# Kernel optimization log

Measured on AMD Instinct MI355X. Metric: run time of the kernel, lower is better.

## Reference

```python
import jax, jax.numpy as jnp
import numpy as np

IN_F, OUT_F = 4096, 14336
F8_MAX = 448.0  # max magnitude of float8_e4m3fn


def setup_inputs() -> dict:
    key = jax.random.key(0)
    kx, kw, kb = jax.random.split(key, 3)
    x = jax.random.normal(kx, (2, 512, IN_F), dtype=jnp.bfloat16)
    w = jax.random.normal(kw, (OUT_F, IN_F), dtype=jnp.float32) * 0.02
    # per-tensor scale: amax / 448 (as in F8Linear.__init__)
    w_scale = (jnp.maximum(jnp.abs(w).max(), 1e-30) / F8_MAX).astype(jnp.float32)
    # quantize to fp8 e4m3; roundtrip back to float32 so the stored values are
    # exactly the fp8-representable values (float32 container keeps the bwd
    # reference's jax.vjp happy while the math is identical)
    w_f8 = jnp.clip(w / w_scale, -F8_MAX, F8_MAX).astype(jnp.float8_e4m3fn).astype(jnp.float32)
    bias = jax.random.normal(kb, (OUT_F,), dtype=jnp.float32) * 0.02
    return {"x": x, "weight_f8": w_f8, "w_scale": w_scale, "bias": bias}


def reference(x, weight_f8, w_scale, bias):
    # dequantize to activation dtype, then GEMM: y = x @ w^T + b
    w = weight_f8.astype(x.dtype) * w_scale.astype(x.dtype)   # [out, in]
    y = jnp.einsum('bsi,oi->bso', x, w) + bias.astype(x.dtype)
    return y
```

## Files before the change

kernel.cpp:

```cpp
#include <hip/hip_runtime.h>
#include <hip/hip_bf16.h>
#include <stdint.h>


#define IN_F   4096
#define OUT_F  14336
#define M_TOT  1024

#define BM 128
#define BN 128
#define BK 32
#define KTILES (IN_F / BK)

typedef __bf16  bf16x8 __attribute__((ext_vector_type(8)));
typedef __bf16  bf16x4 __attribute__((ext_vector_type(4)));
typedef float   f32x4  __attribute__((ext_vector_type(4)));

__device__ __forceinline__ void async_copy16(const void* g, void* l) {
    __builtin_amdgcn_global_load_lds(
        (const __attribute__((address_space(1))) void*)g,
        (__attribute__((address_space(3))) void*)l,
        16, 0, 0);
}

__global__ void detect_x_dtype(const uint32_t* __restrict__ xb,
                               int* __restrict__ flag) {
    __shared__ int any_low;
    if (threadIdx.x == 0) any_low = 0;
    __syncthreads();
    uint32_t bad = 0;
    for (int i = threadIdx.x; i < 1024; i += 256) bad |= (xb[i] & 0xFFFFu);
    if (bad) atomicOr(&any_low, 1);
    __syncthreads();
    if (threadIdx.x == 0) *flag = (any_low == 0) ? 1 : 0;
}

__global__ __launch_bounds__(256) void cvt_w_kernel(
    const f32x4* __restrict__ in, bf16x4* __restrict__ out) {
    const int stride = 3584 * 256;
    for (int i = blockIdx.x * 256 + threadIdx.x; i < 14680064; i += stride) {
        f32x4 v = in[i];
        bf16x4 o;
        o[0] = (__bf16)v[0]; o[1] = (__bf16)v[1];
        o[2] = (__bf16)v[2]; o[3] = (__bf16)v[3];
        out[i] = o;
    }
}

__global__ __launch_bounds__(256) void cvt_x_kernel(
    const void* __restrict__ xraw, bf16x4* __restrict__ out,
    const int* __restrict__ flag) {
    const int f32w = (*flag != 0);
    const int stride = 1024 * 256;
    if (f32w) {
        const f32x4* in = (const f32x4*)xraw;
        for (int i = blockIdx.x * 256 + threadIdx.x; i < 1048576; i += stride) {
            f32x4 v = in[i];
            bf16x4 o;
            o[0] = (__bf16)v[0]; o[1] = (__bf16)v[1];
            o[2] = (__bf16)v[2]; o[3] = (__bf16)v[3];
            out[i] = o;
        }
    } else {
        const bf16x4* in = (const bf16x4*)xraw;
        for (int i = blockIdx.x * 256 + threadIdx.x; i < 1048576; i += stride)
            out[i] = in[i];
    }
}

__global__ __launch_bounds__(256) void gemm_bf16(
    const __bf16* __restrict__ xb,
    const __bf16* __restrict__ wb,
    const float*  __restrict__ w_scale,
    const float*  __restrict__ bias,
    void*         __restrict__ yraw,
    const int*    __restrict__ flag_p)
{
    __shared__ __align__(16) __bf16 As[BM * BK];
    __shared__ __align__(16) __bf16 Bs[BN * BK];

    const int f32w = (*flag_p != 0);

    const int t    = threadIdx.x;
    const int lane = t & 63;
    const int wv   = t >> 6;
    const int wm   = wv >> 1;
    const int wn   = wv & 1;
    const int lidx = lane & 15;
    const int q    = lane >> 4;

    const int flat = blockIdx.x;
    const int xcd  = flat & 7;
    const int slot = flat >> 3;
    const int ni   = xcd * 14 + (slot >> 3);
    const int mi   = slot & 7;
    const int m0   = mi * BM;
    const int n0   = ni * BN;

    const float scale = w_scale[0];

    const int s0 = t, s1 = 256 + t;
    const __bf16* ga0 = xb + (size_t)(m0 + (s0 >> 2)) * IN_F + (s0 & 3) * 8;
    const __bf16* ga1 = xb + (size_t)(m0 + (s1 >> 2)) * IN_F + (s1 & 3) * 8;
    const __bf16* gb0 = wb + (size_t)(n0 + (s0 >> 2)) * IN_F + (s0 & 3) * 8;
    const __bf16* gb1 = wb + (size_t)(n0 + (s1 >> 2)) * IN_F + (s1 & 3) * 8;
    __bf16* la0 = As + s0 * 8;
    __bf16* la1 = As + s1 * 8;
    __bf16* lb0 = Bs + s0 * 8;
    __bf16* lb1 = Bs + s1 * 8;

    const f32x4 zero4 = {0.f, 0.f, 0.f, 0.f};
    f32x4 acc[4][4];
    #pragma unroll
    for (int i = 0; i < 4; ++i)
        #pragma unroll
        for (int j = 0; j < 4; ++j)
            acc[i][j] = zero4;

    for (int kt = 0; kt < KTILES; ++kt) {
        async_copy16(ga0, la0);
        async_copy16(ga1, la1);
        async_copy16(gb0, lb0);
        async_copy16(gb1, lb1);
        ga0 += BK; ga1 += BK; gb0 += BK; gb1 += BK;

        __syncthreads();

        bf16x8 afr[4], bfr[4];
        #pragma unroll
        for (int mt = 0; mt < 4; ++mt) {
            const int row = wm * 64 + mt * 16 + lidx;
            afr[mt] = *reinterpret_cast<const bf16x8*>(As + row * BK + q * 8);
        }
        #pragma unroll
        for (int nt = 0; nt < 4; ++nt) {
            const int row = wn * 64 + nt * 16 + lidx;
            bfr[nt] = *reinterpret_cast<const bf16x8*>(Bs + row * BK + q * 8);
        }

        #pragma unroll
        for (int mt = 0; mt < 4; ++mt)
            #pragma unroll
            for (int nt = 0; nt < 4; ++nt)
                acc[mt][nt] = __builtin_amdgcn_mfma_f32_16x16x32_bf16(
                    afr[mt], bfr[nt], acc[mt][nt], 0, 0, 0);

        __syncthreads();
    }

    float bv[4];
    #pragma unroll
    for (int nt = 0; nt < 4; ++nt)
        bv[nt] = bias[n0 + wn * 64 + nt * 16 + lidx];

    if (f32w) {
        float* yf = (float*)yraw;
        #pragma unroll
        for (int mt = 0; mt < 4; ++mt)
            #pragma unroll
            for (int r = 0; r < 4; ++r) {
                const int m = m0 + wm * 64 + mt * 16 + q * 4 + r;
                float* yp = yf + (size_t)m * OUT_F + n0 + wn * 64 + lidx;
                #pragma unroll
                for (int nt = 0; nt < 4; ++nt)
                    yp[nt * 16] = acc[mt][nt][r] * scale + bv[nt];
            }
    } else {
        __bf16* yh = (__bf16*)yraw;
        #pragma unroll
        for (int mt = 0; mt < 4; ++mt)
            #pragma unroll
            for (int r = 0; r < 4; ++r) {
                const int m = m0 + wm * 64 + mt * 16 + q * 4 + r;
                __bf16* yp = yh + (size_t)m * OUT_F + n0 + wn * 64 + lidx;
                #pragma unroll
                for (int nt = 0; nt < 4; ++nt)
                    yp[nt * 16] = (__bf16)(acc[mt][nt][r] * scale + bv[nt]);
            }
    }
}

__global__ __launch_bounds__(256) void f8linear_fallback(
    const void*  __restrict__ xraw,
    const float* __restrict__ wq,
    const float* __restrict__ w_scale,
    const float* __restrict__ bias,
    void*        __restrict__ yraw,
    const int*   __restrict__ flag_p)
{
    __shared__ __align__(16) __bf16 As[BM * 40];
    __shared__ __align__(16) __bf16 Bs[BN * 40];

    const int f32w = (*flag_p != 0);
    const int t    = threadIdx.x;
    const int lane = t & 63;
    const int wv   = t >> 6;
    const int wm   = wv >> 1;
    const int wn   = wv & 1;
    const int lidx = lane & 15;
    const int q    = lane >> 4;

    const int flat = blockIdx.x;
    const int xcd  = flat & 7;
    const int slot = flat >> 3;
    const int ni   = xcd * 14 + (slot >> 3);
    const int mi   = slot & 7;
    const int m0   = mi * BM;
    const int n0   = ni * BN;

    const float scale = w_scale[0];
    const float*  xf = (const float*)xraw;
    const __bf16* xh = (const __bf16*)xraw;

    const int af_row = t >> 3;
    const int af_col = (t & 7) * 4;
    int ah_row[2], ah_cg[2];
    #pragma unroll
    for (int i = 0; i < 2; ++i) {
        const int s = i * 256 + t;
        ah_row[i] = s >> 2;
        ah_cg[i]  = s & 3;
    }
    const int b_row = t >> 3;
    const int b_col = (t & 7) * 4;

    const f32x4 zero4 = {0.f, 0.f, 0.f, 0.f};
    f32x4 acc[4][4];
    #pragma unroll
    for (int i = 0; i < 4; ++i)
        #pragma unroll
        for (int j = 0; j < 4; ++j)
            acc[i][j] = zero4;

    f32x4  aregf[4];
    bf16x8 aregh[2];
    f32x4  breg[4];
    if (f32w) {
        #pragma unroll
        for (int i = 0; i < 4; ++i)
            aregf[i] = *reinterpret_cast<const f32x4*>(
                xf + (size_t)(m0 + af_row + i * 32) * IN_F + af_col);
    } else {
        #pragma unroll
        for (int i = 0; i < 2; ++i)
            aregh[i] = *reinterpret_cast<const bf16x8*>(
                xh + (size_t)(m0 + ah_row[i]) * IN_F + ah_cg[i] * 8);
    }
    #pragma unroll
    for (int i = 0; i < 4; ++i)
        breg[i] = *reinterpret_cast<const f32x4*>(
            wq + (size_t)(n0 + i * 32 + b_row) * IN_F + b_col);

    for (int kt = 0; kt < KTILES; ++kt) {
        const int k0 = kt * BK;
        if (f32w) {
            #pragma unroll
            for (int i = 0; i < 4; ++i) {
                bf16x4 pk;
                pk[0] = (__bf16)aregf[i][0];
                pk[1] = (__bf16)aregf[i][1];
                pk[2] = (__bf16)aregf[i][2];
                pk[3] = (__bf16)aregf[i][3];
                *reinterpret_cast<bf16x4*>(As + (af_row + i * 32) * 40 + af_col) = pk;
            }
        } else {
            #pragma unroll
            for (int i = 0; i < 2; ++i)
                *reinterpret_cast<bf16x8*>(As + ah_row[i] * 40 + ah_cg[i] * 8) = aregh[i];
        }
        #pragma unroll
        for (int i = 0; i < 4; ++i) {
            bf16x4 pk;
            pk[0] = (__bf16)breg[i][0];
            pk[1] = (__bf16)breg[i][1];
            pk[2] = (__bf16)breg[i][2];
            pk[3] = (__bf16)breg[i][3];
            *reinterpret_cast<bf16x4*>(Bs + (i * 32 + b_row) * 40 + b_col) = pk;
        }
        __syncthreads();
        if (kt + 1 < KTILES) {
            const int k1 = k0 + BK;
            if (f32w) {
                #pragma unroll
                for (int i = 0; i < 4; ++i)
                    aregf[i] = *reinterpret_cast<const f32x4*>(
                        xf + (size_t)(m0 + af_row + i * 32) * IN_F + k1 + af_col);
            } else {
                #pragma unroll
                for (int i = 0; i < 2; ++i)
                    aregh[i] = *reinterpret_cast<const bf16x8*>(
                        xh + (size_t)(m0 + ah_row[i]) * IN_F + k1 + ah_cg[i] * 8);
            }
            #pragma unroll
            for (int i = 0; i < 4; ++i)
                breg[i] = *reinterpret_cast<const f32x4*>(
                    wq + (size_t)(n0 + i * 32 + b_row) * IN_F + k1 + b_col);
        }
        bf16x8 afr[4], bfr[4];
        #pragma unroll
        for (int mt = 0; mt < 4; ++mt) {
            const int row = wm * 64 + mt * 16 + lidx;
            afr[mt] = *reinterpret_cast<const bf16x8*>(As + row * 40 + q * 8);
        }
        #pragma unroll
        for (int nt = 0; nt < 4; ++nt) {
            const int row = wn * 64 + nt * 16 + lidx;
            bfr[nt] = *reinterpret_cast<const bf16x8*>(Bs + row * 40 + q * 8);
        }
        #pragma unroll
        for (int mt = 0; mt < 4; ++mt)
            #pragma unroll
            for (int nt = 0; nt < 4; ++nt)
                acc[mt][nt] = __builtin_amdgcn_mfma_f32_16x16x32_bf16(
                    afr[mt], bfr[nt], acc[mt][nt], 0, 0, 0);
        __syncthreads();
    }

    float bv[4];
    #pragma unroll
    for (int nt = 0; nt < 4; ++nt)
        bv[nt] = bias[n0 + wn * 64 + nt * 16 + lidx];

    if (f32w) {
        float* yf = (float*)yraw;
        #pragma unroll
        for (int mt = 0; mt < 4; ++mt)
            #pragma unroll
            for (int r = 0; r < 4; ++r) {
                const int m = m0 + wm * 64 + mt * 16 + q * 4 + r;
                float* yp = yf + (size_t)m * OUT_F + n0 + wn * 64 + lidx;
                #pragma unroll
                for (int nt = 0; nt < 4; ++nt)
                    yp[nt * 16] = acc[mt][nt][r] * scale + bv[nt];
            }
    } else {
        __bf16* yh = (__bf16*)yraw;
        #pragma unroll
        for (int mt = 0; mt < 4; ++mt)
            #pragma unroll
            for (int r = 0; r < 4; ++r) {
                const int m = m0 + wm * 64 + mt * 16 + q * 4 + r;
                __bf16* yp = yh + (size_t)m * OUT_F + n0 + wn * 64 + lidx;
                #pragma unroll
                for (int nt = 0; nt < 4; ++nt)
                    yp[nt * 16] = (__bf16)(acc[mt][nt][r] * scale + bv[nt]);
            }
    }
}

extern "C" void kernel_launch(void* const* d_in, const int* in_sizes, int n_in,
                              void* d_out, int out_size, void* d_ws, size_t ws_size,
                              hipStream_t stream) {
    const void* px = nullptr; const void* pw = nullptr;
    const void* ps = nullptr; const void* pb = nullptr;
    for (int i = 0; i < n_in; ++i) {
        const long sz = in_sizes[i];
        if      (sz == (long)M_TOT * IN_F) px = d_in[i];
        else if (sz == (long)OUT_F * IN_F) pw = d_in[i];
        else if (sz == 1)                  ps = d_in[i];
        else if (sz == OUT_F)              pb = d_in[i];
    }
    if (!px) px = d_in[0];
    if (!pw) pw = d_in[1];
    if (!ps) ps = d_in[2];
    if (!pb) pb = d_in[3];

    const size_t W_BYTES  = (size_t)OUT_F * IN_F * 2;
    const size_t X_OFF    = W_BYTES;
    const size_t X_BYTES  = (size_t)M_TOT * IN_F * 2;
    const size_t FLAG_OFF = X_OFF + X_BYTES;
    const int grid = (M_TOT / BM) * (OUT_F / BN);

    if (ws_size >= FLAG_OFF + 16) {
        __bf16* wbf  = (__bf16*)d_ws;
        __bf16* xbf  = (__bf16*)((char*)d_ws + X_OFF);
        int*    flag = (int*)((char*)d_ws + FLAG_OFF);

        detect_x_dtype<<<1, 256, 0, stream>>>((const uint32_t*)px, flag);
        cvt_w_kernel<<<3584, 256, 0, stream>>>((const f32x4*)pw, (bf16x4*)wbf);
        cvt_x_kernel<<<1024, 256, 0, stream>>>(px, (bf16x4*)xbf, flag);
        gemm_bf16<<<grid, 256, 0, stream>>>(
            xbf, wbf, (const float*)ps, (const float*)pb, d_out, flag);
    } else {
        int* flag = (int*)d_ws;
        detect_x_dtype<<<1, 256, 0, stream>>>((const uint32_t*)px, flag);
        f8linear_fallback<<<grid, 256, 0, stream>>>(
            px, (const float*)pw, (const float*)ps, (const float*)pb, d_out, flag);
    }
}
```

Baseline: 550.4 us.

## Double GEMM K-tile to 64 with XOR-swizzled LDS and widen conversion kernels

The bf16 GEMM now uses BK=64, halving the number of barrier pairs per K loop. It loads with an XOR swizzle on the 16-byte column groups so that LDS reads are free of bank conflicts. The weight and activation conversion kernels now write 8-wide bf16 vectors, and the x conversion runs one element group per thread with no loop. LDS use doubles to 32KB per block, which may reduce occupancy. The fallback kernel keeps its own 32-wide K step, hardcoded.

```diff
diff --git a/kernel.cpp b/kernel.cpp
--- a/kernel.cpp
+++ b/kernel.cpp
@@ -9,7 +9,7 @@
 
 #define BM 128
 #define BN 128
-#define BK 32
+#define BK 64
 #define KTILES (IN_F / BK)
 
 typedef __bf16  bf16x8 __attribute__((ext_vector_type(8)));
@@ -36,35 +36,37 @@
 }
 
 __global__ __launch_bounds__(256) void cvt_w_kernel(
-    const f32x4* __restrict__ in, bf16x4* __restrict__ out) {
+    const f32x4* __restrict__ in, bf16x8* __restrict__ out) {
     const int stride = 3584 * 256;
-    for (int i = blockIdx.x * 256 + threadIdx.x; i < 14680064; i += stride) {
-        f32x4 v = in[i];
-        bf16x4 o;
-        o[0] = (__bf16)v[0]; o[1] = (__bf16)v[1];
-        o[2] = (__bf16)v[2]; o[3] = (__bf16)v[3];
+    for (int i = blockIdx.x * 256 + threadIdx.x; i < 7340032; i += stride) {
+        f32x4 a = in[2 * i];
+        f32x4 b = in[2 * i + 1];
+        bf16x8 o;
+        o[0] = (__bf16)a[0]; o[1] = (__bf16)a[1];
+        o[2] = (__bf16)a[2]; o[3] = (__bf16)a[3];
+        o[4] = (__bf16)b[0]; o[5] = (__bf16)b[1];
+        o[6] = (__bf16)b[2]; o[7] = (__bf16)b[3];
         out[i] = o;
     }
 }
 
 __global__ __launch_bounds__(256) void cvt_x_kernel(
-    const void* __restrict__ xraw, bf16x4* __restrict__ out,
+    const void* __restrict__ xraw, bf16x8* __restrict__ out,
     const int* __restrict__ flag) {
     const int f32w = (*flag != 0);
-    const int stride = 1024 * 256;
+    const int i = blockIdx.x * 256 + threadIdx.x;
     if (f32w) {
         const f32x4* in = (const f32x4*)xraw;
-        for (int i = blockIdx.x * 256 + threadIdx.x; i < 1048576; i += stride) {
-            f32x4 v = in[i];
-            bf16x4 o;
-            o[0] = (__bf16)v[0]; o[1] = (__bf16)v[1];
-            o[2] = (__bf16)v[2]; o[3] = (__bf16)v[3];
-            out[i] = o;
-        }
+        f32x4 a = in[2 * i];
+        f32x4 b = in[2 * i + 1];
+        bf16x8 o;
+        o[0] = (__bf16)a[0]; o[1] = (__bf16)a[1];
+        o[2] = (__bf16)a[2]; o[3] = (__bf16)a[3];
+        o[4] = (__bf16)b[0]; o[5] = (__bf16)b[1];
+        o[6] = (__bf16)b[2]; o[7] = (__bf16)b[3];
+        out[i] = o;
     } else {
-        const bf16x4* in = (const bf16x4*)xraw;
-        for (int i = blockIdx.x * 256 + threadIdx.x; i < 1048576; i += stride)
-            out[i] = in[i];
+        out[i] = ((const bf16x8*)xraw)[i];
     }
 }
 
@@ -99,15 +101,18 @@
 
     const float scale = w_scale[0];
 
-    const int s0 = t, s1 = 256 + t;
-    const __bf16* ga0 = xb + (size_t)(m0 + (s0 >> 2)) * IN_F + (s0 & 3) * 8;
-    const __bf16* ga1 = xb + (size_t)(m0 + (s1 >> 2)) * IN_F + (s1 & 3) * 8;
-    const __bf16* gb0 = wb + (size_t)(n0 + (s0 >> 2)) * IN_F + (s0 & 3) * 8;
-    const __bf16* gb1 = wb + (size_t)(n0 + (s1 >> 2)) * IN_F + (s1 & 3) * 8;
-    __bf16* la0 = As + s0 * 8;
-    __bf16* la1 = As + s1 * 8;
-    __bf16* lb0 = Bs + s0 * 8;
-    __bf16* lb1 = Bs + s1 * 8;
+    const __bf16* ga[4]; const __bf16* gb[4];
+    __bf16* la[4]; __bf16* lb[4];
+    #pragma unroll
+    for (int i = 0; i < 4; ++i) {
+        const int s   = i * 256 + t;
+        const int row = s >> 3;
+        const int cgl = (s & 7) ^ (row & 7);
+        ga[i] = xb + (size_t)(m0 + row) * IN_F + cgl * 8;
+        gb[i] = wb + (size_t)(n0 + row) * IN_F + cgl * 8;
+        la[i] = As + s * 8;
+        lb[i] = Bs + s * 8;
+    }
 
     const f32x4 zero4 = {0.f, 0.f, 0.f, 0.f};
     f32x4 acc[4][4];
@@ -118,32 +123,37 @@
             acc[i][j] = zero4;
 
     for (int kt = 0; kt < KTILES; ++kt) {
-        async_copy16(ga0, la0);
-        async_copy16(ga1, la1);
-        async_copy16(gb0, lb0);
-        async_copy16(gb1, lb1);
-        ga0 += BK; ga1 += BK; gb0 += BK; gb1 += BK;
+        #pragma unroll
+        for (int i = 0; i < 4; ++i) {
+            async_copy16(ga[i], la[i]);
+            async_copy16(gb[i], lb[i]);
+            ga[i] += BK; gb[i] += BK;
+        }
 
         __syncthreads();
 
-        bf16x8 afr[4], bfr[4];
-        #pragma unroll
-        for (int mt = 0; mt < 4; ++mt) {
-            const int row = wm * 64 + mt * 16 + lidx;
-            afr[mt] = *reinterpret_cast<const bf16x8*>(As + row * BK + q * 8);
-        }
-        #pragma unroll
-        for (int nt = 0; nt < 4; ++nt) {
-            const int row = wn * 64 + nt * 16 + lidx;
-            bfr[nt] = *reinterpret_cast<const bf16x8*>(Bs + row * BK + q * 8);
-        }
-
-        #pragma unroll
-        for (int mt = 0; mt < 4; ++mt)
-            #pragma unroll
-            for (int nt = 0; nt < 4; ++nt)
-                acc[mt][nt] = __builtin_amdgcn_mfma_f32_16x16x32_bf16(
-                    afr[mt], bfr[nt], acc[mt][nt], 0, 0, 0);
+        #pragma unroll
+        for (int ko = 0; ko < 2; ++ko) {
+            bf16x8 afr[4], bfr[4];
+            #pragma unroll
+            for (int mt = 0; mt < 4; ++mt) {
+                const int row = wm * 64 + mt * 16 + lidx;
+                const int cgp = (ko * 4 + q) ^ (row & 7);
+                afr[mt] = *reinterpret_cast<const bf16x8*>(As + row * BK + cgp * 8);
+            }
+            #pragma unroll
+            for (int nt = 0; nt < 4; ++nt) {
+                const int row = wn * 64 + nt * 16 + lidx;
+                const int cgp = (ko * 4 + q) ^ (row & 7);
+                bfr[nt] = *reinterpret_cast<const bf16x8*>(Bs + row * BK + cgp * 8);
+            }
+            #pragma unroll
+            for (int mt = 0; mt < 4; ++mt)
+                #pragma unroll
+                for (int nt = 0; nt < 4; ++nt)
+                    acc[mt][nt] = __builtin_amdgcn_mfma_f32_16x16x32_bf16(
+                        afr[mt], bfr[nt], acc[mt][nt], 0, 0, 0);
+        }
 
         __syncthreads();
     }
@@ -251,8 +261,8 @@
         breg[i] = *reinterpret_cast<const f32x4*>(
             wq + (size_t)(n0 + i * 32 + b_row) * IN_F + b_col);
 
-    for (int kt = 0; kt < KTILES; ++kt) {
-        const int k0 = kt * BK;
+    for (int kt = 0; kt < 128; ++kt) {
+        const int k0 = kt * 32;
         if (f32w) {
             #pragma unroll
             for (int i = 0; i < 4; ++i) {
@@ -278,8 +288,8 @@
             *reinterpret_cast<bf16x4*>(Bs + (i * 32 + b_row) * 40 + b_col) = pk;
         }
         __syncthreads();
-        if (kt + 1 < KTILES) {
-            const int k1 = k0 + BK;
+        if (kt + 1 < 128) {
+            const int k1 = k0 + 32;
             if (f32w) {
                 #pragma unroll
                 for (int i = 0; i < 4; ++i)
@@ -377,8 +387,8 @@
         int*    flag = (int*)((char*)d_ws + FLAG_OFF);
 
         detect_x_dtype<<<1, 256, 0, stream>>>((const uint32_t*)px, flag);
-        cvt_w_kernel<<<3584, 256, 0, stream>>>((const f32x4*)pw, (bf16x4*)wbf);
-        cvt_x_kernel<<<1024, 256, 0, stream>>>(px, (bf16x4*)xbf, flag);
+        cvt_w_kernel<<<3584, 256, 0, stream>>>((const f32x4*)pw, (bf16x8*)wbf);
+        cvt_x_kernel<<<2048, 256, 0, stream>>>(px, (bf16x8*)xbf, flag);
         gemm_bf16<<<grid, 256, 0, stream>>>(
             xbf, wbf, (const float*)ps, (const float*)pb, d_out, flag);
     } else {
```

Result: faster. 532.1 us (-3.3%).
